# Kernel tuning notes

Hardware: AMD Instinct MI355X
Metric: run time of the kernel (lower is better)

## Reference

```python
import jax, jax.numpy as jnp
import numpy as np

N = 50000
E = 800000
D_IN = 128
D_H = 128
D_OUT = 1


def setup_inputs() -> dict:
    key = jax.random.key(0)
    ks = jax.random.split(key, 12)
    x = jax.random.normal(ks[0], (N, D_IN), dtype=jnp.float32)
    edge_index = jax.random.randint(ks[1], (2, E), 0, N, dtype=jnp.int64)
    def glorot(k, shape):
        lim = float(np.sqrt(6.0 / (shape[0] + shape[1])))
        return jax.random.uniform(k, shape, jnp.float32, -lim, lim)
    return {
        "x": x,
        "edge_index": edge_index,
        "W1": glorot(ks[2], (D_IN, D_H)),  "b1": jnp.zeros((D_H,), jnp.float32),
        "W2": glorot(ks[3], (D_H, D_H)),   "b2": jnp.zeros((D_H,), jnp.float32),
        "W3": glorot(ks[4], (D_H, D_H)),   "b3": jnp.zeros((D_H,), jnp.float32),
        "Wfc": glorot(ks[5], (D_H, D_OUT)), "bfc": jnp.zeros((D_OUT,), jnp.float32),
    }


def _gcn_norm(edge_index, num_nodes):
    # Add self-loops (PyG GCNConv default) and compute symmetric normalization
    loops = jnp.arange(num_nodes, dtype=edge_index.dtype)
    src = jnp.concatenate([edge_index[0], loops])
    dst = jnp.concatenate([edge_index[1], loops])
    ones = jnp.ones(src.shape[0], dtype=jnp.float32)
    deg = jax.ops.segment_sum(ones, dst, num_segments=num_nodes)
    dinv = jnp.where(deg > 0, jax.lax.rsqrt(deg), 0.0)
    norm = dinv[src] * dinv[dst]  # [E + N]
    return src, dst, norm


def _gcn_layer(x, W, b, src, dst, norm, num_nodes):
    xw = x @ W                              # [N, out] dense transform first
    msg = xw[src] * norm[:, None]           # gather + scale
    agg = jax.ops.segment_sum(msg, dst, num_segments=num_nodes)  # scatter-add
    return agg + b


def reference(x, edge_index, W1, b1, W2, b2, W3, b3, Wfc, bfc):
    num_nodes = x.shape[0]
    src, dst, norm = _gcn_norm(edge_index, num_nodes)
    h = jax.nn.relu(_gcn_layer(x, W1, b1, src, dst, norm, num_nodes))
    h = jax.nn.relu(_gcn_layer(h, W2, b2, src, dst, norm, num_nodes))
    h = jax.nn.relu(_gcn_layer(h, W3, b3, src, dst, norm, num_nodes))
    return h @ Wfc + bfc  # [N, 1]
```

## Files before the change

### kernel.cpp

```cpp
#include <hip/hip_runtime.h>

#define D 128
#define SCAN_ELEMS 4096

typedef __attribute__((ext_vector_type(8))) short short8;
typedef __attribute__((ext_vector_type(4))) float f32x4;


__global__ void count_kernel(const int* __restrict__ dst, int* __restrict__ deg,
                             int* __restrict__ rank, int e) {
    int i = blockIdx.x * blockDim.x + threadIdx.x;
    if (i < e) rank[i] = atomicAdd(&deg[dst[i]], 1);
}

__global__ __launch_bounds__(256) void scanA_kernel(const int* __restrict__ deg,
                                                    int* __restrict__ blkSums, int n) {
    __shared__ int waveSums[4];
    int t = threadIdx.x;
    int base = blockIdx.x * SCAN_ELEMS + t * 16;
    int s = 0;
    if (base + 16 <= n) {
        const int4* p = reinterpret_cast<const int4*>(deg + base);
        #pragma unroll
        for (int k = 0; k < 4; ++k) {
            int4 v = p[k];
            s += v.x + v.y + v.z + v.w;
        }
    } else {
        for (int k = 0; k < 16; ++k) {
            int i = base + k;
            if (i < n) s += deg[i];
        }
    }
    #pragma unroll
    for (int off = 32; off > 0; off >>= 1) s += __shfl_down(s, off);
    int lane = t & 63, w = t >> 6;
    if (lane == 0) waveSums[w] = s;
    __syncthreads();
    if (t == 0) blkSums[blockIdx.x] = waveSums[0] + waveSums[1] + waveSums[2] + waveSums[3];
}

__global__ __launch_bounds__(256) void scanC_kernel(const int* __restrict__ deg,
                                                    const int* __restrict__ blkSums,
                                                    int* __restrict__ offsets,
                                                    float* __restrict__ dinv, int n, int nblk) {
    __shared__ int waveSums[4];
    __shared__ int blkBase;
    int t = threadIdx.x;
    int lane = t & 63, w = t >> 6;

    if (t < 64) {
        int s = (t < nblk && t < blockIdx.x) ? blkSums[t] : 0;
        #pragma unroll
        for (int off = 32; off > 0; off >>= 1) s += __shfl_down(s, off);
        if (t == 0) blkBase = s;
    }

    int base = blockIdx.x * SCAN_ELEMS + t * 16;
    int v[16];
    int s = 0;
    #pragma unroll
    for (int k = 0; k < 16; ++k) {
        int i = base + k;
        int d = (i < n) ? deg[i] : 0;
        v[k] = d;
        s += d;
    }
    int incl = s;
    #pragma unroll
    for (int off = 1; off < 64; off <<= 1) {
        int u = __shfl_up(incl, off);
        if (lane >= off) incl += u;
    }
    if (lane == 63) waveSums[w] = incl;
    __syncthreads();
    int waveOff = 0;
    for (int i = 0; i < 4; ++i) if (i < w) waveOff += waveSums[i];
    int off0 = blkBase + waveOff + incl - s;

    #pragma unroll
    for (int k = 0; k < 16; ++k) {
        int i = base + k;
        if (i < n) {
            offsets[i] = off0;
            dinv[i] = rsqrtf((float)(v[k] + 1));
            off0 += v[k];
        }
    }
}

__global__ void fill_kernel(const int* __restrict__ src, const int* __restrict__ dst,
                            const int* __restrict__ offsets, const int* __restrict__ rank,
                            int* __restrict__ csr_src, int e) {
    int i = blockIdx.x * blockDim.x + threadIdx.x;
    if (i < e) {
        csr_src[offsets[dst[i]] + rank[i]] = src[i];
    }
}

__device__ inline void f2bf(float f, short& hi, short& lo) {
    union { float f; unsigned u; } a; a.f = f;
    unsigned r = a.u + 0x7fffu + ((a.u >> 16) & 1u);
    hi = (short)(r >> 16);
    union { unsigned u; float f; } h; h.u = ((unsigned)(unsigned short)hi) << 16;
    union { float f; unsigned u; } b; b.f = f - h.f;
    unsigned r2 = b.u + 0x7fffu + ((b.u >> 16) & 1u);
    lo = (short)(r2 >> 16);
}

__global__ __launch_bounds__(256) void wsplit_kernel(const float* __restrict__ W1,
                                                     const float* __restrict__ W2,
                                                     const float* __restrict__ W3,
                                                     short* __restrict__ Bsw) {
    int tid = blockIdx.x * 256 + threadIdx.x;
    int layer = tid >> 14;
    int rem = tid & 16383;
    int k = rem >> 7, c = rem & 127;
    const float* Wg = (layer == 0) ? W1 : ((layer == 1) ? W2 : W3);
    float v = Wg[k * 128 + c];
    short hi, lo; f2bf(v, hi, lo);
    int ktile = k >> 5, kk = k & 31, q = kk >> 3, j = kk & 7;
    int ct = c >> 4, mm = c & 15, lane = q * 16 + mm;
    int idx = layer * 32768 + ((ktile * 8 + ct) * 64 + lane) * 8 + j;
    Bsw[idx] = hi;
    Bsw[idx + 16384] = lo;
}

__global__ __launch_bounds__(256) void gemm_kernel(const float* __restrict__ A,
                                                   const short* __restrict__ Bsw,
                                                   const float* __restrict__ dinv,
                                                   float* __restrict__ outp, int n) {
    int t = threadIdx.x;
    int w = t >> 6;
    int lane = t & 63;
    int quad = lane >> 4;
    int m = lane & 15;

    int rowBase = blockIdx.x * 64 + w * 16;
    int arow = rowBase + m;
    bool valid = arow < n;
    const float* ap = A + (size_t)(valid ? arow : 0) * D + quad * 8;

    f32x4 acc[8];
    #pragma unroll
    for (int ct = 0; ct < 8; ++ct) acc[ct] = (f32x4){0.f, 0.f, 0.f, 0.f};

    #pragma unroll
    for (int kt = 0; kt < 4; ++kt) {
        short8 a_hi, a_lo;
        {
            float4 f0 = *reinterpret_cast<const float4*>(ap + kt * 32);
            float4 f1 = *reinterpret_cast<const float4*>(ap + kt * 32 + 4);
            float fv[8] = {f0.x, f0.y, f0.z, f0.w, f1.x, f1.y, f1.z, f1.w};
            #pragma unroll
            for (int j = 0; j < 8; ++j) {
                short h, l; f2bf(valid ? fv[j] : 0.f, h, l);
                a_hi[j] = h; a_lo[j] = l;
            }
        }
        const short* bp = Bsw + (kt * 8 * 64 + lane) * 8;
        #pragma unroll
        for (int ct = 0; ct < 8; ++ct) {
            short8 b_hi = *reinterpret_cast<const short8*>(bp + ct * 512);
            short8 b_lo = *reinterpret_cast<const short8*>(bp + 16384 + ct * 512);
            acc[ct] = __builtin_amdgcn_mfma_f32_16x16x32_bf16(a_hi, b_hi, acc[ct], 0, 0, 0);
            acc[ct] = __builtin_amdgcn_mfma_f32_16x16x32_bf16(a_hi, b_lo, acc[ct], 0, 0, 0);
            acc[ct] = __builtin_amdgcn_mfma_f32_16x16x32_bf16(a_lo, b_hi, acc[ct], 0, 0, 0);
        }
    }

    #pragma unroll
    for (int r = 0; r < 4; ++r) {
        int orow = rowBase + quad * 4 + r;
        if (orow < n) {
            float s = dinv[orow];
            float* o = outp + (size_t)orow * D + m;
            #pragma unroll
            for (int ct = 0; ct < 8; ++ct) o[ct * 16] = acc[ct][r] * s;
        }
    }
}

__global__ __launch_bounds__(256) void agg_kernel(const float* __restrict__ xws,
                                                  const int* __restrict__ csr_src,
                                                  const int* __restrict__ offsets,
                                                  const int* __restrict__ deg,
                                                  const float* __restrict__ dinv,
                                                  const float* __restrict__ bias,
                                                  float* __restrict__ outp,
                                                  const float* __restrict__ fcw,
                                                  const float* __restrict__ fcb,
                                                  float* __restrict__ fcout,
                                                  int n) {
    int wave = (blockIdx.x * blockDim.x + threadIdx.x) >> 6;
    int lane = threadIdx.x & 63;
    if (wave >= n) return;
    int node = wave;
    int half = lane >> 5;
    int l32  = lane & 31;
    size_t col = (size_t)(l32 << 2);

    int base = offsets[node];
    int cnt  = deg[node];

    float di = dinv[node];
    float4 vs = *reinterpret_cast<const float4*>(xws + (size_t)node * D + col);
    float4 b  = *reinterpret_cast<const float4*>(bias + col);

    float4 acc0 = make_float4(0.f, 0.f, 0.f, 0.f);
    float4 acc1 = make_float4(0.f, 0.f, 0.f, 0.f);
    float4 acc2 = make_float4(0.f, 0.f, 0.f, 0.f);
    float4 acc3 = make_float4(0.f, 0.f, 0.f, 0.f);

    if (cnt <= 64) {
        int idx = (lane < cnt) ? csr_src[base + lane] : 0;
        int j = 0;
        for (; j + 8 <= cnt; j += 8) {
            int s0 = __shfl(idx, j     + half);
            int s1 = __shfl(idx, j + 2 + half);
            int s2 = __shfl(idx, j + 4 + half);
            int s3 = __shfl(idx, j + 6 + half);
            float4 v0 = *reinterpret_cast<const float4*>(xws + (size_t)s0 * D + col);
            float4 v1 = *reinterpret_cast<const float4*>(xws + (size_t)s1 * D + col);
            float4 v2 = *reinterpret_cast<const float4*>(xws + (size_t)s2 * D + col);
            float4 v3 = *reinterpret_cast<const float4*>(xws + (size_t)s3 * D + col);
            acc0.x += v0.x; acc0.y += v0.y; acc0.z += v0.z; acc0.w += v0.w;
            acc1.x += v1.x; acc1.y += v1.y; acc1.z += v1.z; acc1.w += v1.w;
            acc2.x += v2.x; acc2.y += v2.y; acc2.z += v2.z; acc2.w += v2.w;
            acc3.x += v3.x; acc3.y += v3.y; acc3.z += v3.z; acc3.w += v3.w;
        }
        for (; j + 2 <= cnt; j += 2) {
            int s0 = __shfl(idx, j + half);
            float4 v0 = *reinterpret_cast<const float4*>(xws + (size_t)s0 * D + col);
            acc0.x += v0.x; acc0.y += v0.y; acc0.z += v0.z; acc0.w += v0.w;
        }
        if (j < cnt) {
            int s0 = __shfl(idx, j);
            if (half == 0) {
                float4 v0 = *reinterpret_cast<const float4*>(xws + (size_t)s0 * D + col);
                acc1.x += v0.x; acc1.y += v0.y; acc1.z += v0.z; acc1.w += v0.w;
            }
        }
    } else {
        int j = 0;
        for (; j + 2 <= cnt; j += 2) {
            int s = csr_src[base + j + half];
            float4 v = *reinterpret_cast<const float4*>(xws + (size_t)s * D + col);
            acc0.x += v.x; acc0.y += v.y; acc0.z += v.z; acc0.w += v.w;
        }
        if (j < cnt && half == 0) {
            int s = csr_src[base + j];
            float4 v = *reinterpret_cast<const float4*>(xws + (size_t)s * D + col);
            acc1.x += v.x; acc1.y += v.y; acc1.z += v.z; acc1.w += v.w;
        }
    }

    acc0.x += acc1.x + acc2.x + acc3.x;
    acc0.y += acc1.y + acc2.y + acc3.y;
    acc0.z += acc1.z + acc2.z + acc3.z;
    acc0.w += acc1.w + acc2.w + acc3.w;
    acc0.x += __shfl_down(acc0.x, 32);
    acc0.y += __shfl_down(acc0.y, 32);
    acc0.z += __shfl_down(acc0.z, 32);
    acc0.w += __shfl_down(acc0.w, 32);

    float4 r;
    r.x = fmaxf(di * (acc0.x + vs.x) + b.x, 0.f);
    r.y = fmaxf(di * (acc0.y + vs.y) + b.y, 0.f);
    r.z = fmaxf(di * (acc0.z + vs.z) + b.z, 0.f);
    r.w = fmaxf(di * (acc0.w + vs.w) + b.w, 0.f);

    if (fcw == nullptr) {
        if (half == 0)
            *reinterpret_cast<float4*>(outp + (size_t)node * D + col) = r;
    } else {
        float4 wv = *reinterpret_cast<const float4*>(fcw + col);
        float s = (half == 0) ? (r.x * wv.x + r.y * wv.y + r.z * wv.z + r.w * wv.w) : 0.f;
        #pragma unroll
        for (int off = 32; off > 0; off >>= 1) s += __shfl_down(s, off);
        if (lane == 0) fcout[node] = s + fcb[0];
    }
}


extern "C" void kernel_launch(void* const* d_in, const int* in_sizes, int n_in,
                              void* d_out, int out_size, void* d_ws, size_t ws_size,
                              hipStream_t stream) {
    const float* x   = (const float*)d_in[0];
    const int*   ei  = (const int*)d_in[1];
    const float* W1  = (const float*)d_in[2];
    const float* b1  = (const float*)d_in[3];
    const float* W2  = (const float*)d_in[4];
    const float* b2  = (const float*)d_in[5];
    const float* W3  = (const float*)d_in[6];
    const float* b3  = (const float*)d_in[7];
    const float* Wfc = (const float*)d_in[8];
    const float* bfc = (const float*)d_in[9];
    float* outp = (float*)d_out;

    const int n = in_sizes[0] / D;
    const int e = in_sizes[1] / 2;
    const int* src = ei;
    const int* dst = ei + e;

    char* ws = (char*)d_ws;
    size_t off = 0;
    auto alloc = [&](size_t bytes) {
        void* p = ws + off;
        off += (bytes + 255) & ~(size_t)255;
        return p;
    };
    int*   deg     = (int*)alloc((size_t)n * 4);
    size_t zero_bytes = off;
    int*   offsets = (int*)alloc((size_t)n * 4);
    float* dinv    = (float*)alloc((size_t)n * 4);
    int*   blkSums = (int*)alloc(64 * 4);
    short* Bsw     = (short*)alloc((size_t)3 * 32768 * 2);
    int*   rank    = (int*)alloc((size_t)e * 4);
    int*   csr_src = (int*)alloc((size_t)e * 4);
    float* buf0    = (float*)alloc((size_t)n * D * 4);
    float* buf1    = (float*)alloc((size_t)n * D * 4);

    int eb256 = (e + 255) / 256;
    int scan_blocks = (n + SCAN_ELEMS - 1) / SCAN_ELEMS;

    hipMemsetAsync(ws, 0, zero_bytes, stream);
    count_kernel <<<eb256, 256, 0, stream>>>(dst, deg, rank, e);
    scanA_kernel <<<scan_blocks, 256, 0, stream>>>(deg, blkSums, n);
    scanC_kernel <<<scan_blocks, 256, 0, stream>>>(deg, blkSums, offsets, dinv, n, scan_blocks);
    fill_kernel  <<<eb256, 256, 0, stream>>>(src, dst, offsets, rank, csr_src, e);
    wsplit_kernel<<<192, 256, 0, stream>>>(W1, W2, W3, Bsw);

    int gemm_blocks = (n + 63) / 64;
    int agg_blocks  = (n + 3) / 4;

    gemm_kernel<<<gemm_blocks, 256, 0, stream>>>(x, Bsw, dinv, buf0, n);
    agg_kernel <<<agg_blocks, 256, 0, stream>>>(buf0, csr_src, offsets, deg, dinv, b1, buf1,
                                                nullptr, nullptr, nullptr, n);
    gemm_kernel<<<gemm_blocks, 256, 0, stream>>>(buf1, Bsw + 32768, dinv, buf0, n);
    agg_kernel <<<agg_blocks, 256, 0, stream>>>(buf0, csr_src, offsets, deg, dinv, b2, buf1,
                                                nullptr, nullptr, nullptr, n);
    gemm_kernel<<<gemm_blocks, 256, 0, stream>>>(buf1, Bsw + 65536, dinv, buf0, n);
    agg_kernel <<<agg_blocks, 256, 0, stream>>>(buf0, csr_src, offsets, deg, dinv, b3, nullptr,
                                                Wfc, bfc, outp, n);
}
```

Measured before the change: 364.3 us.

## Store GEMM output as split 24-bit floats to shrink aggregation gathers

The GEMM epilogue stages results through shared memory and encodes each float as a rounded 24-bit value. The top 16 bits go to one array and the low 8 bits to a separate byte array, with coalesced vector stores. The aggregation kernel gathers these narrower rows and rebuilds floats, which cuts gather bytes per neighbour by a quarter. The cost is extra encode/decode ALU work, an LDS round-trip with a barrier, and a loss of mantissa precision that stays within tolerance.

```diff
diff --git a/kernel.cpp b/kernel.cpp
--- a/kernel.cpp
+++ b/kernel.cpp
@@ -106,6 +106,12 @@
     union { float f; unsigned u; } b; b.f = f - h.f;
     unsigned r2 = b.u + 0x7fffu + ((b.u >> 16) & 1u);
     lo = (short)(r2 >> 16);
+}
+
+__device__ inline unsigned enc24(float f) {
+    union { float f; unsigned u; } a; a.f = f;
+    unsigned r = a.u + 0x7fu + ((a.u >> 8) & 1u);
+    return r >> 8;
 }
 
 __global__ __launch_bounds__(256) void wsplit_kernel(const float* __restrict__ W1,
@@ -129,7 +135,10 @@
 __global__ __launch_bounds__(256) void gemm_kernel(const float* __restrict__ A,
                                                    const short* __restrict__ Bsw,
                                                    const float* __restrict__ dinv,
-                                                   float* __restrict__ outp, int n) {
+                                                   unsigned short* __restrict__ xh,
+                                                   unsigned char* __restrict__ xl, int n) {
+    __shared__ float tile[4][16][132];
+
     int t = threadIdx.x;
     int w = t >> 6;
     int lane = t & 63;
@@ -172,16 +181,53 @@
     #pragma unroll
     for (int r = 0; r < 4; ++r) {
         int orow = rowBase + quad * 4 + r;
-        if (orow < n) {
-            float s = dinv[orow];
-            float* o = outp + (size_t)orow * D + m;
-            #pragma unroll
-            for (int ct = 0; ct < 8; ++ct) o[ct * 16] = acc[ct][r] * s;
-        }
-    }
-}
-
-__global__ __launch_bounds__(256) void agg_kernel(const float* __restrict__ xws,
+        float s = (orow < n) ? dinv[orow] : 0.f;
+        #pragma unroll
+        for (int ct = 0; ct < 8; ++ct)
+            tile[w][quad * 4 + r][m + ct * 16] = acc[ct][r] * s;
+    }
+    __syncthreads();
+
+    int r = lane >> 2;
+    int c0 = (lane & 3) << 5;
+    int gr = rowBase + r;
+    if (gr < n) {
+        unsigned hu[16], lu[8];
+        #pragma unroll
+        for (int g = 0; g < 8; ++g) {
+            float4 f = *reinterpret_cast<const float4*>(&tile[w][r][c0 + g * 4]);
+            unsigned e0 = enc24(f.x), e1 = enc24(f.y), e2 = enc24(f.z), e3 = enc24(f.w);
+            hu[g * 2]     = (e0 >> 8) | ((e1 >> 8) << 16);
+            hu[g * 2 + 1] = (e2 >> 8) | ((e3 >> 8) << 16);
+            lu[g] = (e0 & 0xffu) | ((e1 & 0xffu) << 8) | ((e2 & 0xffu) << 16) | ((e3 & 0xffu) << 24);
+        }
+        uint4* hp = reinterpret_cast<uint4*>(xh + (size_t)gr * 128 + c0);
+        uint4* lp = reinterpret_cast<uint4*>(xl + (size_t)gr * 128 + c0);
+        hp[0] = *reinterpret_cast<uint4*>(&hu[0]);
+        hp[1] = *reinterpret_cast<uint4*>(&hu[4]);
+        hp[2] = *reinterpret_cast<uint4*>(&hu[8]);
+        hp[3] = *reinterpret_cast<uint4*>(&hu[12]);
+        lp[0] = *reinterpret_cast<uint4*>(&lu[0]);
+        lp[1] = *reinterpret_cast<uint4*>(&lu[4]);
+    }
+}
+
+
+__device__ inline void g24(const unsigned short* __restrict__ xh,
+                           const unsigned char* __restrict__ xl,
+                           int row, int c, float4& a) {
+    uint2 h2 = *reinterpret_cast<const uint2*>(xh + (size_t)row * 128 + c);
+    unsigned lb = *reinterpret_cast<const unsigned*>(xl + (size_t)row * 128 + c);
+    union { unsigned u; float f; } v0, v1, v2, v3;
+    v0.u = ((h2.x & 0xffffu) << 16) | ((lb & 0xffu) << 8);
+    v1.u = (h2.x & 0xffff0000u)     | (((lb >> 8) & 0xffu) << 8);
+    v2.u = ((h2.y & 0xffffu) << 16) | (((lb >> 16) & 0xffu) << 8);
+    v3.u = (h2.y & 0xffff0000u)     | ((lb >> 24) << 8);
+    a.x += v0.f; a.y += v1.f; a.z += v2.f; a.w += v3.f;
+}
+
+__global__ __launch_bounds__(256) void agg_kernel(const unsigned short* __restrict__ xh,
+                                                  const unsigned char* __restrict__ xl,
                                                   const int* __restrict__ csr_src,
                                                   const int* __restrict__ offsets,
                                                   const int* __restrict__ deg,
@@ -198,14 +244,15 @@
     int node = wave;
     int half = lane >> 5;
     int l32  = lane & 31;
-    size_t col = (size_t)(l32 << 2);
+    int col  = l32 << 2;
 
     int base = offsets[node];
     int cnt  = deg[node];
 
     float di = dinv[node];
-    float4 vs = *reinterpret_cast<const float4*>(xws + (size_t)node * D + col);
-    float4 b  = *reinterpret_cast<const float4*>(bias + col);
+    float4 vs = make_float4(0.f, 0.f, 0.f, 0.f);
+    g24(xh, xl, node, col, vs);
+    float4 b = *reinterpret_cast<const float4*>(bias + col);
 
     float4 acc0 = make_float4(0.f, 0.f, 0.f, 0.f);
     float4 acc1 = make_float4(0.f, 0.f, 0.f, 0.f);
@@ -220,38 +267,28 @@
             int s1 = __shfl(idx, j + 2 + half);
             int s2 = __shfl(idx, j + 4 + half);
             int s3 = __shfl(idx, j + 6 + half);
-            float4 v0 = *reinterpret_cast<const float4*>(xws + (size_t)s0 * D + col);
-            float4 v1 = *reinterpret_cast<const float4*>(xws + (size_t)s1 * D + col);
-            float4 v2 = *reinterpret_cast<const float4*>(xws + (size_t)s2 * D + col);
-            float4 v3 = *reinterpret_cast<const float4*>(xws + (size_t)s3 * D + col);
-            acc0.x += v0.x; acc0.y += v0.y; acc0.z += v0.z; acc0.w += v0.w;
-            acc1.x += v1.x; acc1.y += v1.y; acc1.z += v1.z; acc1.w += v1.w;
-            acc2.x += v2.x; acc2.y += v2.y; acc2.z += v2.z; acc2.w += v2.w;
-            acc3.x += v3.x; acc3.y += v3.y; acc3.z += v3.z; acc3.w += v3.w;
+            g24(xh, xl, s0, col, acc0);
+            g24(xh, xl, s1, col, acc1);
+            g24(xh, xl, s2, col, acc2);
+            g24(xh, xl, s3, col, acc3);
         }
         for (; j + 2 <= cnt; j += 2) {
             int s0 = __shfl(idx, j + half);
-            float4 v0 = *reinterpret_cast<const float4*>(xws + (size_t)s0 * D + col);
-            acc0.x += v0.x; acc0.y += v0.y; acc0.z += v0.z; acc0.w += v0.w;
+            g24(xh, xl, s0, col, acc0);
         }
         if (j < cnt) {
             int s0 = __shfl(idx, j);
-            if (half == 0) {
-                float4 v0 = *reinterpret_cast<const float4*>(xws + (size_t)s0 * D + col);
-                acc1.x += v0.x; acc1.y += v0.y; acc1.z += v0.z; acc1.w += v0.w;
-            }
+            if (half == 0) g24(xh, xl, s0, col, acc1);
         }
     } else {
         int j = 0;
         for (; j + 2 <= cnt; j += 2) {
             int s = csr_src[base + j + half];
-            float4 v = *reinterpret_cast<const float4*>(xws + (size_t)s * D + col);
-            acc0.x += v.x; acc0.y += v.y; acc0.z += v.z; acc0.w += v.w;
+            g24(xh, xl, s, col, acc0);
         }
         if (j < cnt && half == 0) {
             int s = csr_src[base + j];
-            float4 v = *reinterpret_cast<const float4*>(xws + (size_t)s * D + col);
-            acc1.x += v.x; acc1.y += v.y; acc1.z += v.z; acc1.w += v.w;
+            g24(xh, xl, s, col, acc1);
         }
     }
 
@@ -310,16 +347,17 @@
         off += (bytes + 255) & ~(size_t)255;
         return p;
     };
-    int*   deg     = (int*)alloc((size_t)n * 4);
-    size_t zero_bytes = off;
-    int*   offsets = (int*)alloc((size_t)n * 4);
-    float* dinv    = (float*)alloc((size_t)n * 4);
-    int*   blkSums = (int*)alloc(64 * 4);
-    short* Bsw     = (short*)alloc((size_t)3 * 32768 * 2);
-    int*   rank    = (int*)alloc((size_t)e * 4);
-    int*   csr_src = (int*)alloc((size_t)e * 4);
-    float* buf0    = (float*)alloc((size_t)n * D * 4);
-    float* buf1    = (float*)alloc((size_t)n * D * 4);
+    int*            deg     = (int*)alloc((size_t)n * 4);
+    size_t          zero_bytes = off;
+    int*            offsets = (int*)alloc((size_t)n * 4);
+    float*          dinv    = (float*)alloc((size_t)n * 4);
+    int*            blkSums = (int*)alloc(64 * 4);
+    short*          Bsw     = (short*)alloc((size_t)3 * 32768 * 2);
+    int*            rank    = (int*)alloc((size_t)e * 4);
+    int*            csr_src = (int*)alloc((size_t)e * 4);
+    unsigned short* xhbuf   = (unsigned short*)alloc((size_t)n * 128 * 2);
+    unsigned char*  xlbuf   = (unsigned char*)alloc((size_t)n * 128);
+    float*          buf1    = (float*)alloc((size_t)n * D * 4);
 
     int eb256 = (e + 255) / 256;
     int scan_blocks = (n + SCAN_ELEMS - 1) / SCAN_ELEMS;
@@ -334,13 +372,13 @@
     int gemm_blocks = (n + 63) / 64;
     int agg_blocks  = (n + 3) / 4;
 
-    gemm_kernel<<<gemm_blocks, 256, 0, stream>>>(x, Bsw, dinv, buf0, n);
-    agg_kernel <<<agg_blocks, 256, 0, stream>>>(buf0, csr_src, offsets, deg, dinv, b1, buf1,
+    gemm_kernel<<<gemm_blocks, 256, 0, stream>>>(x, Bsw, dinv, xhbuf, xlbuf, n);
+    agg_kernel <<<agg_blocks, 256, 0, stream>>>(xhbuf, xlbuf, csr_src, offsets, deg, dinv, b1, buf1,
                                                 nullptr, nullptr, nullptr, n);
-    gemm_kernel<<<gemm_blocks, 256, 0, stream>>>(buf1, Bsw + 32768, dinv, buf0, n);
-    agg_kernel <<<agg_blocks, 256, 0, stream>>>(buf0, csr_src, offsets, deg, dinv, b2, buf1,
+    gemm_kernel<<<gemm_blocks, 256, 0, stream>>>(buf1, Bsw + 32768, dinv, xhbuf, xlbuf, n);
+    agg_kernel <<<agg_blocks, 256, 0, stream>>>(xhbuf, xlbuf, csr_src, offsets, deg, dinv, b2, buf1,
                                                 nullptr, nullptr, nullptr, n);
-    gemm_kernel<<<gemm_blocks, 256, 0, stream>>>(buf1, Bsw + 65536, dinv, buf0, n);
-    agg_kernel <<<agg_blocks, 256, 0, stream>>>(buf0, csr_src, offsets, deg, dinv, b3, nullptr,
+    gemm_kernel<<<gemm_blocks, 256, 0, stream>>>(buf1, Bsw + 65536, dinv, xhbuf, xlbuf, n);
+    agg_kernel <<<agg_blocks, 256, 0, stream>>>(xhbuf, xlbuf, csr_src, offsets, deg, dinv, b3, nullptr,
                                                 Wfc, bfc, outp, n);
 }
```

Result: faster. 334.8 us (-8.1%).
